# Optimization experiments

Measured on AMD Instinct MI355X. Metric: run time of the kernel, lower is better.

## Reference

```python
import math
import jax, jax.numpy as jnp
import numpy as np

MODEL_DIM = 4096
NUM_EXPERTS = 64
NUM_TOKENS = 8192
CAPACITY_FACTOR = 1.0


def setup_inputs() -> dict:
    key = jax.random.key(0)
    kx, kw = jax.random.split(key)
    x = jax.random.normal(kx, (NUM_TOKENS, MODEL_DIM), dtype=jnp.float32)
    # nn.Linear weight: [num_experts, model_dim]
    W = jax.random.normal(kw, (NUM_EXPERTS, MODEL_DIM), dtype=jnp.float32) * (1.0 / math.sqrt(MODEL_DIM))
    return {"x": x, "W": W}


def reference(x, W):
    # gating projection (no bias), cast to fp32 as in top1gating
    logits = jnp.matmul(x, W.T).astype(jnp.float32)  # [S, E]
    num_tokens, num_experts = logits.shape
    capacity = int(CAPACITY_FACTOR * math.ceil(num_tokens / num_experts))

    indices1_s = jnp.argmax(logits, axis=1)                        # [S]
    gates = jax.nn.softmax(logits, axis=1)                         # [S, E]
    mask1 = jax.nn.one_hot(indices1_s, num_experts, dtype=jnp.float32)  # [S, E]
    gates1_s = jnp.sum(gates * mask1, axis=1)                      # [S]
    # per-expert running position of each routed token
    locations1 = jnp.cumsum(mask1, axis=0) - 1.0                   # [S, E]
    locations1_s = jnp.sum(locations1 * mask1, axis=1)             # [S]

    return (indices1_s.astype(jnp.int32),
            capacity,
            locations1_s.astype(jnp.int32),
            gates1_s,
            num_experts)
```

## Files before the change

### kernel.cpp

```cpp
#include <hip/hip_runtime.h>
#include <math.h>

#define NTOK 8192
#define MDIM 4096
#define NEXP 64
#define CAPACITY 128.0f

#define OFF_IDX  0
#define OFF_CAP  8192
#define OFF_LOC  8193
#define OFF_GATE 16385
#define OFF_NE   24577

#define KC 32

#define NCHK 256

#define WS_CNT_OFF  0
#define WS_RK_OFF   16384
#define WS_SB_OFF   24576
#define WS_W_OFF    40960
#define WS_PART_OFF (40960 + (3 * NEXP * MDIM) / 2)

using bf16x8 = __attribute__((ext_vector_type(8))) short;
using f32x4  = __attribute__((ext_vector_type(4))) float;

static __device__ __forceinline__ unsigned short f2bf(float f) {
    union { float f; unsigned u; } v; v.f = f;
    unsigned r = v.u + 0x7fffu + ((v.u >> 16) & 1u);
    return (unsigned short)(r >> 16);
}
static __device__ __forceinline__ float bf2f(unsigned short h) {
    union { unsigned u; float f; } v; v.u = ((unsigned)h) << 16;
    return v.f;
}

__global__ __launch_bounds__(256) void prep_w(
    const float* __restrict__ W, unsigned short* __restrict__ Ws)
{
    const int gid = blockIdx.x * 256 + threadIdx.x;
    const int e   = gid >> 10;
    const int f4  = gid & 1023;
    float4 v = ((const float4*)W)[e * 1024 + f4];
    float av[4] = {v.x, v.y, v.z, v.w};
    unsigned short h[3][4];
    #pragma unroll
    for (int j = 0; j < 4; ++j) {
        float a = av[j];
        unsigned short b1 = f2bf(a);  float r1 = a  - bf2f(b1);
        unsigned short b2 = f2bf(r1); float r2 = r1 - bf2f(b2);
        unsigned short b3 = f2bf(r2);
        h[0][j] = b1; h[1][j] = b2; h[2][j] = b3;
    }
    #pragma unroll
    for (int t = 0; t < 3; ++t)
        *(ushort4*)&Ws[((size_t)(t * 64 + e)) * MDIM + f4 * 4] =
            make_ushort4(h[t][0], h[t][1], h[t][2], h[t][3]);
}

template<int S>
__global__ __launch_bounds__(64, 3) void gate_mfma(
    const float* __restrict__ x,
    const unsigned short* __restrict__ Ws,
    float* __restrict__ part)
{
    constexpr int KSL = MDIM / S;
    constexpr int NCH = KSL / KC;

    __shared__ __align__(16) float4 xs[2][32][8];

    const int lane  = threadIdx.x & 63;
    const int m     = lane & 15;
    const int g     = lane >> 4;
    const int tok0  = blockIdx.x * 32;
    const int slice = blockIdx.y;
    const int k0    = slice * KSL;

    const float4* __restrict__ x4 = (const float4*)x;
    const unsigned short* __restrict__ wp =
        Ws + (size_t)m * MDIM + k0 + g * 8;

    auto stage = [&](int c, int b) {
        #pragma unroll
        for (int j = 0; j < 4; ++j) {
            const int row  = j * 8 + (lane >> 3);
            const int srcs = (lane & 7) ^ (row & 7);
            const float4* gsrc = x4 + (size_t)(tok0 + row) * (MDIM / 4)
                                 + (k0 >> 2) + c * 8 + srcs;
            void* ldst = (void*)&xs[b][j * 8][0];
            __builtin_amdgcn_global_load_lds(
                (const __attribute__((address_space(1))) void*)gsrc,
                (__attribute__((address_space(3))) void*)ldst, 16, 0, 0);
        }
    };

    auto cvt = [&](float4 lo, float4 hi, bf16x8& r0, bf16x8& r1, bf16x8& r2) {
        float f[8] = {lo.x, lo.y, lo.z, lo.w, hi.x, hi.y, hi.z, hi.w};
        #pragma unroll
        for (int j = 0; j < 8; ++j) {
            float a = f[j];
            unsigned short b1 = f2bf(a);  float t1 = a  - bf2f(b1);
            unsigned short b2 = f2bf(t1); float t2 = t1 - bf2f(b2);
            unsigned short b3 = f2bf(t2);
            r0[j] = (short)b1; r1[j] = (short)b2; r2[j] = (short)b3;
        }
    };

    f32x4 acc[2][4];
    #pragma unroll
    for (int gr = 0; gr < 2; ++gr)
        #pragma unroll
        for (int nt = 0; nt < 4; ++nt) acc[gr][nt] = (f32x4){0.f, 0.f, 0.f, 0.f};

    stage(0, 0);

    for (int c = 0; c < NCH; ++c) {
        const int cur = c & 1;

        bf16x8 w[3][4];
        const unsigned short* q = wp + c * KC;
        #pragma unroll
        for (int t = 0; t < 3; ++t)
            #pragma unroll
            for (int nt = 0; nt < 4; ++nt)
                w[t][nt] = *(const bf16x8*)(q + (size_t)(t * 64 + nt * 16) * MDIM);

        if (c + 1 < NCH) stage(c + 1, cur ^ 1);

        bf16x8 a[2][3];
        #pragma unroll
        for (int gr = 0; gr < 2; ++gr) {
            const int row = gr * 16 + m;
            float4 lo = xs[cur][row][(2 * g    ) ^ (m & 7)];
            float4 hi = xs[cur][row][(2 * g + 1) ^ (m & 7)];
            cvt(lo, hi, a[gr][0], a[gr][1], a[gr][2]);
        }

        #pragma unroll
        for (int gr = 0; gr < 2; ++gr)
            #pragma unroll
            for (int nt = 0; nt < 4; ++nt)
                acc[gr][nt] = __builtin_amdgcn_mfma_f32_16x16x32_bf16(a[gr][2], w[0][nt], acc[gr][nt], 0, 0, 0);
        #pragma unroll
        for (int gr = 0; gr < 2; ++gr)
            #pragma unroll
            for (int nt = 0; nt < 4; ++nt)
                acc[gr][nt] = __builtin_amdgcn_mfma_f32_16x16x32_bf16(a[gr][0], w[2][nt], acc[gr][nt], 0, 0, 0);
        #pragma unroll
        for (int gr = 0; gr < 2; ++gr)
            #pragma unroll
            for (int nt = 0; nt < 4; ++nt)
                acc[gr][nt] = __builtin_amdgcn_mfma_f32_16x16x32_bf16(a[gr][1], w[1][nt], acc[gr][nt], 0, 0, 0);
        #pragma unroll
        for (int gr = 0; gr < 2; ++gr)
            #pragma unroll
            for (int nt = 0; nt < 4; ++nt)
                acc[gr][nt] = __builtin_amdgcn_mfma_f32_16x16x32_bf16(a[gr][1], w[0][nt], acc[gr][nt], 0, 0, 0);
        #pragma unroll
        for (int gr = 0; gr < 2; ++gr)
            #pragma unroll
            for (int nt = 0; nt < 4; ++nt)
                acc[gr][nt] = __builtin_amdgcn_mfma_f32_16x16x32_bf16(a[gr][0], w[1][nt], acc[gr][nt], 0, 0, 0);
        #pragma unroll
        for (int gr = 0; gr < 2; ++gr)
            #pragma unroll
            for (int nt = 0; nt < 4; ++nt)
                acc[gr][nt] = __builtin_amdgcn_mfma_f32_16x16x32_bf16(a[gr][0], w[0][nt], acc[gr][nt], 0, 0, 0);
    }

    #pragma unroll
    for (int gr = 0; gr < 2; ++gr)
        #pragma unroll
        for (int nt = 0; nt < 4; ++nt)
            #pragma unroll
            for (int r = 0; r < 4; ++r) {
                const int tokr = tok0 + gr * 16 + g * 4 + r;
                part[((size_t)slice * NTOK + tokr) * 64 + nt * 16 + m] = acc[gr][nt][r];
            }
}

template<int S>
__global__ __launch_bounds__(256) void reduce_count(
    const float* __restrict__ part,
    float* __restrict__ out,
    int* __restrict__ cnt,
    int* __restrict__ rk)
{
    __shared__ int eidx[32];

    const int tid  = threadIdx.x;
    const int tok0 = blockIdx.x * 32;
    const int trel = tid >> 3;
    const int tok  = tok0 + trel;
    const int q    = tid & 7;

    const float4* __restrict__ p4 = (const float4*)part;

    float4 a[2];
    #pragma unroll
    for (int r = 0; r < 2; ++r) a[r] = make_float4(0.f, 0.f, 0.f, 0.f);
    for (int s = 0; s < S; ++s) {
        #pragma unroll
        for (int r = 0; r < 2; ++r) {
            float4 v = p4[((size_t)s * NTOK + tok) * 16 + q * 2 + r];
            a[r].x += v.x; a[r].y += v.y; a[r].z += v.z; a[r].w += v.w;
        }
    }

    float vals[8] = {a[0].x, a[0].y, a[0].z, a[0].w,
                     a[1].x, a[1].y, a[1].z, a[1].w};

    float bm = vals[0];
    int   be = q * 8;
    #pragma unroll
    for (int j = 1; j < 8; ++j)
        if (vals[j] > bm) { bm = vals[j]; be = q * 8 + j; }
    #pragma unroll
    for (int off = 1; off <= 4; off <<= 1) {
        float om = __shfl_xor(bm, off, 64);
        int   oe = __shfl_xor(be, off, 64);
        if (om > bm || (om == bm && oe < be)) { bm = om; be = oe; }
    }

    float es = 0.f;
    #pragma unroll
    for (int j = 0; j < 8; ++j) es += expf(vals[j] - bm);
    #pragma unroll
    for (int off = 1; off <= 4; off <<= 1)
        es += __shfl_xor(es, off, 64);

    if (q == 0) {
        out[OFF_IDX  + tok] = (float)be;
        out[OFF_GATE + tok] = 1.0f / es;
        eidx[trel] = be;
    }
    __syncthreads();

    if (tid < 64) {
        const int e = (tid < 32) ? eidx[tid] : -1;
        const unsigned long long lt =
            (tid == 0) ? 0ull : ((~0ull) >> (64 - tid));
        unsigned long long mymask = 0;
        int myrk = 0;
        for (int ee = 0; ee < 64; ++ee) {
            unsigned long long mb = __ballot(e == ee);
            if (tid == ee) mymask = mb;
            if (e == ee)   myrk   = (int)__popcll(mb & lt);
        }
        cnt[blockIdx.x * 64 + tid] = (int)__popcll(mymask);
        if (tid < 32) rk[tok0 + tid] = myrk;
    }
    if (tid == 0 && blockIdx.x == 0) {
        out[OFF_CAP] = CAPACITY;
        out[OFF_NE]  = (float)NEXP;
    }
}

__global__ __launch_bounds__(64) void scan_e(
    const int* __restrict__ cnt, int* __restrict__ sb)
{
    const int e = blockIdx.x;
    const int l = threadIdx.x & 63;

    int v[4], s[4];
    #pragma unroll
    for (int seg = 0; seg < 4; ++seg)
        v[seg] = cnt[(seg * 64 + l) * 64 + e];

    #pragma unroll
    for (int seg = 0; seg < 4; ++seg) {
        int sv = v[seg];
        #pragma unroll
        for (int off = 1; off <= 32; off <<= 1) {
            int u = __shfl_up(sv, off, 64);
            if (l >= off) sv += u;
        }
        s[seg] = sv;
    }
    int t0 = __shfl(s[0], 63, 64);
    int t1 = __shfl(s[1], 63, 64);
    int t2 = __shfl(s[2], 63, 64);
    s[1] += t0; s[2] += t0 + t1; s[3] += t0 + t1 + t2;

    #pragma unroll
    for (int seg = 0; seg < 4; ++seg)
        sb[(seg * 64 + l) * 64 + e] = s[seg] - v[seg];
}

__global__ __launch_bounds__(256) void emit_loc(
    const float* __restrict__ idxf,
    const int* __restrict__ sb,
    const int* __restrict__ rk,
    float* __restrict__ out)
{
    const int s = blockIdx.x * 256 + threadIdx.x;
    const int e = (int)idxf[s];
    out[OFF_LOC + s] = (float)(sb[(s >> 5) * 64 + e] + rk[s]);
}

extern "C" void kernel_launch(void* const* d_in, const int* in_sizes, int n_in,
                              void* d_out, int out_size, void* d_ws, size_t ws_size,
                              hipStream_t stream)
{
    const float* x = (const float*)d_in[0];
    const float* W = (const float*)d_in[1];
    float* out = (float*)d_out;

    int*   cnt  = (int*)d_ws + WS_CNT_OFF;
    int*   rk   = (int*)d_ws + WS_RK_OFF;
    int*   sb   = (int*)d_ws + WS_SB_OFF;
    unsigned short* Ws = (unsigned short*)((int*)d_ws + WS_W_OFF);
    float* part = (float*)d_ws + WS_PART_OFF;

    prep_w<<<256, 256, 0, stream>>>(W, Ws);

    const size_t base = (size_t)WS_PART_OFF * 4;
    const size_t per_slice = (size_t)NTOK * 64 * 4;

    if (ws_size >= base + 16 * per_slice) {
        gate_mfma<16><<<dim3(256, 16), 64, 0, stream>>>(x, Ws, part);
        reduce_count<16><<<256, 256, 0, stream>>>(part, out, cnt, rk);
    } else if (ws_size >= base + 8 * per_slice) {
        gate_mfma<8><<<dim3(256, 8), 64, 0, stream>>>(x, Ws, part);
        reduce_count<8><<<256, 256, 0, stream>>>(part, out, cnt, rk);
    } else if (ws_size >= base + 4 * per_slice) {
        gate_mfma<4><<<dim3(256, 4), 64, 0, stream>>>(x, Ws, part);
        reduce_count<4><<<256, 256, 0, stream>>>(part, out, cnt, rk);
    } else if (ws_size >= base + 2 * per_slice) {
        gate_mfma<2><<<dim3(256, 2), 64, 0, stream>>>(x, Ws, part);
        reduce_count<2><<<256, 256, 0, stream>>>(part, out, cnt, rk);
    } else {
        gate_mfma<1><<<dim3(256, 1), 64, 0, stream>>>(x, Ws, part);
        reduce_count<1><<<256, 256, 0, stream>>>(part, out, cnt, rk);
    }

    scan_e<<<64, 64, 0, stream>>>(cnt, sb);
    emit_loc<<<32, 256, 0, stream>>>(out + OFF_IDX, sb, rk, out);
}
```

Measured before the change: 260.1 us.

## Fuse weight split into GEMM via LDS, merge scan and location emit

Drops the separate prep_w kernel. Each 512-thread block now loads its K-slice of W, splits it into three bf16 parts and stores them swizzled in LDS, where 8 waves share them. The x staging changes from a double buffer to a single per-wave buffer, with the next stage issued after the current values are read. scan_e and emit_loc are merged into one single-block kernel, removing launches and a workspace round trip at the cost of a serial single-block scan and more LDS per block.

```diff
diff --git a/kernel.cpp b/kernel.cpp
--- a/kernel.cpp
+++ b/kernel.cpp
@@ -12,15 +12,14 @@
 #define OFF_GATE 16385
 #define OFF_NE   24577
 
-#define KC 32
-
-#define NCHK 256
+#define NSLICE 16
+#define KSL    (MDIM / NSLICE)
+#define KC     32
+#define NCH    (KSL / KC)
 
 #define WS_CNT_OFF  0
 #define WS_RK_OFF   16384
-#define WS_SB_OFF   24576
-#define WS_W_OFF    40960
-#define WS_PART_OFF (40960 + (3 * NEXP * MDIM) / 2)
+#define WS_PART_OFF 24576
 
 using bf16x8 = __attribute__((ext_vector_type(8))) short;
 using f32x4  = __attribute__((ext_vector_type(4))) float;
@@ -35,64 +34,67 @@
     return v.f;
 }
 
-__global__ __launch_bounds__(256) void prep_w(
-    const float* __restrict__ W, unsigned short* __restrict__ Ws)
-{
-    const int gid = blockIdx.x * 256 + threadIdx.x;
-    const int e   = gid >> 10;
-    const int f4  = gid & 1023;
-    float4 v = ((const float4*)W)[e * 1024 + f4];
-    float av[4] = {v.x, v.y, v.z, v.w};
-    unsigned short h[3][4];
-    #pragma unroll
-    for (int j = 0; j < 4; ++j) {
-        float a = av[j];
-        unsigned short b1 = f2bf(a);  float r1 = a  - bf2f(b1);
-        unsigned short b2 = f2bf(r1); float r2 = r1 - bf2f(b2);
-        unsigned short b3 = f2bf(r2);
-        h[0][j] = b1; h[1][j] = b2; h[2][j] = b3;
-    }
-    #pragma unroll
-    for (int t = 0; t < 3; ++t)
-        *(ushort4*)&Ws[((size_t)(t * 64 + e)) * MDIM + f4 * 4] =
-            make_ushort4(h[t][0], h[t][1], h[t][2], h[t][3]);
-}
-
-template<int S>
-__global__ __launch_bounds__(64, 3) void gate_mfma(
+__global__ __launch_bounds__(512, 2) void gate_mfma(
     const float* __restrict__ x,
-    const unsigned short* __restrict__ Ws,
+    const float* __restrict__ W,
     float* __restrict__ part)
 {
-    constexpr int KSL = MDIM / S;
-    constexpr int NCH = KSL / KC;
-
-    __shared__ __align__(16) float4 xs[2][32][8];
-
-    const int lane  = threadIdx.x & 63;
+    __shared__ __align__(16) unsigned short wl[NCH * 3][64][32];
+    __shared__ __align__(16) float4 xs[8][32][8];
+
+    const int tid   = threadIdx.x;
+    const int lane  = tid & 63;
+    const int wv    = tid >> 6;
     const int m     = lane & 15;
     const int g     = lane >> 4;
-    const int tok0  = blockIdx.x * 32;
+    const int tok0  = blockIdx.x * 256 + wv * 32;
     const int slice = blockIdx.y;
     const int k0    = slice * KSL;
 
     const float4* __restrict__ x4 = (const float4*)x;
-    const unsigned short* __restrict__ wp =
-        Ws + (size_t)m * MDIM + k0 + g * 8;
-
-    auto stage = [&](int c, int b) {
+
+    auto stage = [&](int c) {
         #pragma unroll
         for (int j = 0; j < 4; ++j) {
             const int row  = j * 8 + (lane >> 3);
             const int srcs = (lane & 7) ^ (row & 7);
             const float4* gsrc = x4 + (size_t)(tok0 + row) * (MDIM / 4)
                                  + (k0 >> 2) + c * 8 + srcs;
-            void* ldst = (void*)&xs[b][j * 8][0];
+            void* ldst = (void*)&xs[wv][j * 8][0];
             __builtin_amdgcn_global_load_lds(
                 (const __attribute__((address_space(1))) void*)gsrc,
                 (__attribute__((address_space(3))) void*)ldst, 16, 0, 0);
         }
     };
+
+    stage(0);
+
+    #pragma unroll
+    for (int r = 0; r < 8; ++r) {
+        const int j4  = r * 512 + tid;
+        const int e   = j4 >> 6;
+        const int kk4 = j4 & 63;
+        float4 v = *(const float4*)(W + (size_t)e * MDIM + k0 + kk4 * 4);
+        const int c    = kk4 >> 3;
+        const int slog = (kk4 >> 1) & 3;
+        const int half = kk4 & 1;
+        const int phys = slog ^ ((e >> 1) & 3);
+        float av[4] = {v.x, v.y, v.z, v.w};
+        unsigned short h[3][4];
+        #pragma unroll
+        for (int j = 0; j < 4; ++j) {
+            float a = av[j];
+            unsigned short b1 = f2bf(a);  float t1 = a  - bf2f(b1);
+            unsigned short b2 = f2bf(t1); float t2 = t1 - bf2f(b2);
+            unsigned short b3 = f2bf(t2);
+            h[0][j] = b1; h[1][j] = b2; h[2][j] = b3;
+        }
+        #pragma unroll
+        for (int t = 0; t < 3; ++t)
+            *(ushort4*)&wl[c * 3 + t][e][phys * 8 + half * 4] =
+                make_ushort4(h[t][0], h[t][1], h[t][2], h[t][3]);
+    }
+    __syncthreads();
 
     auto cvt = [&](float4 lo, float4 hi, bf16x8& r0, bf16x8& r1, bf16x8& r2) {
         float f[8] = {lo.x, lo.y, lo.z, lo.w, hi.x, hi.y, hi.z, hi.w};
@@ -112,29 +114,28 @@
         #pragma unroll
         for (int nt = 0; nt < 4; ++nt) acc[gr][nt] = (f32x4){0.f, 0.f, 0.f, 0.f};
 
-    stage(0, 0);
-
     for (int c = 0; c < NCH; ++c) {
-        const int cur = c & 1;
-
         bf16x8 w[3][4];
-        const unsigned short* q = wp + c * KC;
         #pragma unroll
         for (int t = 0; t < 3; ++t)
             #pragma unroll
-            for (int nt = 0; nt < 4; ++nt)
-                w[t][nt] = *(const bf16x8*)(q + (size_t)(t * 64 + nt * 16) * MDIM);
-
-        if (c + 1 < NCH) stage(c + 1, cur ^ 1);
+            for (int nt = 0; nt < 4; ++nt) {
+                const int e    = nt * 16 + m;
+                const int phys = g ^ ((e >> 1) & 3);
+                w[t][nt] = *(const bf16x8*)&wl[c * 3 + t][e][phys * 8];
+            }
 
         bf16x8 a[2][3];
         #pragma unroll
         for (int gr = 0; gr < 2; ++gr) {
             const int row = gr * 16 + m;
-            float4 lo = xs[cur][row][(2 * g    ) ^ (m & 7)];
-            float4 hi = xs[cur][row][(2 * g + 1) ^ (m & 7)];
+            float4 lo = xs[wv][row][(2 * g    ) ^ (m & 7)];
+            float4 hi = xs[wv][row][(2 * g + 1) ^ (m & 7)];
             cvt(lo, hi, a[gr][0], a[gr][1], a[gr][2]);
         }
+
+        __builtin_amdgcn_sched_barrier(0);
+        if (c + 1 < NCH) stage(c + 1);
 
         #pragma unroll
         for (int gr = 0; gr < 2; ++gr)
@@ -256,46 +257,50 @@
     }
 }
 
-__global__ __launch_bounds__(64) void scan_e(
-    const int* __restrict__ cnt, int* __restrict__ sb)
-{
-    const int e = blockIdx.x;
-    const int l = threadIdx.x & 63;
-
-    int v[4], s[4];
-    #pragma unroll
-    for (int seg = 0; seg < 4; ++seg)
-        v[seg] = cnt[(seg * 64 + l) * 64 + e];
-
-    #pragma unroll
-    for (int seg = 0; seg < 4; ++seg) {
-        int sv = v[seg];
-        #pragma unroll
-        for (int off = 1; off <= 32; off <<= 1) {
-            int u = __shfl_up(sv, off, 64);
-            if (l >= off) sv += u;
-        }
-        s[seg] = sv;
-    }
-    int t0 = __shfl(s[0], 63, 64);
-    int t1 = __shfl(s[1], 63, 64);
-    int t2 = __shfl(s[2], 63, 64);
-    s[1] += t0; s[2] += t0 + t1; s[3] += t0 + t1 + t2;
-
-    #pragma unroll
-    for (int seg = 0; seg < 4; ++seg)
-        sb[(seg * 64 + l) * 64 + e] = s[seg] - v[seg];
-}
-
-__global__ __launch_bounds__(256) void emit_loc(
+__global__ __launch_bounds__(512) void scan_emit(
     const float* __restrict__ idxf,
-    const int* __restrict__ sb,
+    const int* __restrict__ cnt,
     const int* __restrict__ rk,
     float* __restrict__ out)
 {
-    const int s = blockIdx.x * 256 + threadIdx.x;
-    const int e = (int)idxf[s];
-    out[OFF_LOC + s] = (float)(sb[(s >> 5) * 64 + e] + rk[s]);
+    __shared__ int sc[256][64];
+    __shared__ int ps[64][8];
+
+    const int tid = threadIdx.x;
+    const int e   = tid >> 3;
+    const int q   = tid & 7;
+
+    #pragma unroll
+    for (int r = 0; r < 32; ++r) sc[0][r * 512 + tid] = cnt[r * 512 + tid];
+    __syncthreads();
+
+    {
+        int sum = 0;
+        #pragma unroll
+        for (int j = 0; j < 32; ++j) sum += sc[q * 32 + j][e];
+        ps[e][q] = sum;
+    }
+    __syncthreads();
+
+    {
+        int base = 0;
+        for (int qq = 0; qq < 8; ++qq) { if (qq < q) base += ps[e][qq]; }
+        #pragma unroll
+        for (int j = 0; j < 32; ++j) {
+            int ch = q * 32 + j;
+            int v  = sc[ch][e];
+            sc[ch][e] = base;
+            base += v;
+        }
+    }
+    __syncthreads();
+
+    #pragma unroll
+    for (int r = 0; r < 16; ++r) {
+        const int s  = r * 512 + tid;
+        const int ee = (int)idxf[s];
+        out[OFF_LOC + s] = (float)(sc[s >> 5][ee] + rk[s]);
+    }
 }
 
 extern "C" void kernel_launch(void* const* d_in, const int* in_sizes, int n_in,
@@ -308,32 +313,9 @@
 
     int*   cnt  = (int*)d_ws + WS_CNT_OFF;
     int*   rk   = (int*)d_ws + WS_RK_OFF;
-    int*   sb   = (int*)d_ws + WS_SB_OFF;
-    unsigned short* Ws = (unsigned short*)((int*)d_ws + WS_W_OFF);
     float* part = (float*)d_ws + WS_PART_OFF;
 
-    prep_w<<<256, 256, 0, stream>>>(W, Ws);
-
-    const size_t base = (size_t)WS_PART_OFF * 4;
-    const size_t per_slice = (size_t)NTOK * 64 * 4;
-
-    if (ws_size >= base + 16 * per_slice) {
-        gate_mfma<16><<<dim3(256, 16), 64, 0, stream>>>(x, Ws, part);
-        reduce_count<16><<<256, 256, 0, stream>>>(part, out, cnt, rk);
-    } else if (ws_size >= base + 8 * per_slice) {
-        gate_mfma<8><<<dim3(256, 8), 64, 0, stream>>>(x, Ws, part);
-        reduce_count<8><<<256, 256, 0, stream>>>(part, out, cnt, rk);
-    } else if (ws_size >= base + 4 * per_slice) {
-        gate_mfma<4><<<dim3(256, 4), 64, 0, stream>>>(x, Ws, part);
-        reduce_count<4><<<256, 256, 0, stream>>>(part, out, cnt, rk);
-    } else if (ws_size >= base + 2 * per_slice) {
-        gate_mfma<2><<<dim3(256, 2), 64, 0, stream>>>(x, Ws, part);
-        reduce_count<2><<<256, 256, 0, stream>>>(part, out, cnt, rk);
-    } else {
-        gate_mfma<1><<<dim3(256, 1), 64, 0, stream>>>(x, Ws, part);
-        reduce_count<1><<<256, 256, 0, stream>>>(part, out, cnt, rk);
-    }
-
-    scan_e<<<64, 64, 0, stream>>>(cnt, sb);
-    emit_loc<<<32, 256, 0, stream>>>(out + OFF_IDX, sb, rk, out);
-}
+    gate_mfma<<<dim3(32, NSLICE), 512, 0, stream>>>(x, W, part);
+    reduce_count<NSLICE><<<256, 256, 0, stream>>>(part, out, cnt, rk);
+    scan_emit<<<1, 512, 0, stream>>>(out + OFF_IDX, cnt, rk, out);
+}
```

After: 227.8 us. 1.14x faster.
